# Performance work log

Measured on AMD Instinct MI355X. Metric: run time of the kernel, lower is better.

## Reference

```python
import jax, jax.numpy as jnp
import numpy as np
import math

# dims (see shape_source)
B, S, D, H, DH, W, L, F = 2, 4096, 768, 12, 64, 256, 4, 2048
DV, DID, NIN, V, CD, CS = 256, 32, 8, 4, 16, 64
DEMB = CD * CS
EPS = 1e-6
NEG = -1e9


def rmsnorm(x, w):
    y = x * jax.lax.rsqrt(jnp.mean(x * x, axis=-1, keepdims=True) + EPS)
    return y * w


def sliding_attn(q, k, v):
    # q,k,v: [B,H,S,DH]; banded attention, each query attends keys within +-W.
    nc = S // W
    q = q * (1.0 / math.sqrt(DH))
    kp = jnp.pad(k, ((0, 0), (0, 0), (W, W), (0, 0)))
    vp = jnp.pad(v, ((0, 0), (0, 0), (W, W), (0, 0)))
    idx = jnp.arange(nc)[:, None] * W + jnp.arange(3 * W)[None, :]  # [nc,3W] into padded seq
    kc = kp[:, :, idx]                                # [B,H,nc,3W,DH]
    vc = vp[:, :, idx]
    qc = q.reshape(B, H, nc, W, DH)
    scores = jnp.einsum('bhcqd,bhckd->bhcqk', qc, kc)  # [B,H,nc,W,3W]
    qpos = jnp.arange(W)[:, None]
    kpos = jnp.arange(3 * W)[None, :]
    band = jnp.abs(kpos - (qpos + W)) <= W             # [W,3W]
    kglob = jnp.arange(nc)[:, None, None] * W + kpos[None] - W  # [nc,1,3W]
    valid = band[None] & (kglob >= 0) & (kglob < S)    # [nc,W,3W]
    scores = jnp.where(valid[None, None], scores, NEG)
    probs = jax.nn.softmax(scores, axis=-1)
    out = jnp.einsum('bhcqk,bhckd->bhcqd', probs, vc)
    return out.reshape(B, H, S, DH)


def _forward(x, id, embed_table, cd_w, cd_b, wq, bq, wk, bk, wv, bv,
             attn_norm_w, ffn_norm_w, w1, b1, w2, b2, w3, b3,
             h0_w1, h0_b1, h0_w2, h0_b2, norm_head0_w, head0_w, head0_b,
             c1_w1, c1_b1, c1_w2, c1_b2, c2_w1, c2_b1, c2_w2, c2_b2,
             norm_emb_w, head1_w, head1_b):
    h = embed_table[x] * math.sqrt(DV)                         # [B,S,DV]
    bits = jnp.arange(DID - 1, -1, -1)
    idb = ((id[..., None] >> bits) & 1).astype(jnp.float32)    # decimal2binary -> [B,S,DID]
    h = jnp.concatenate([h, idb], axis=-1) @ cd_w + cd_b       # correct_dim -> [B,S,D]
    for l in range(L):
        a = rmsnorm(h, attn_norm_w[l])
        q = (a @ wq[l] + bq[l]).reshape(B, S, H, DH).transpose(0, 2, 1, 3)
        k = (a @ wk[l] + bk[l]).reshape(B, S, H, DH).transpose(0, 2, 1, 3)
        v = (a @ wv[l] + bv[l]).reshape(B, S, H, DH).transpose(0, 2, 1, 3)
        o = sliding_attn(q, k, v)                              # [B,H,S,DH]
        h = h + o.transpose(0, 2, 1, 3).reshape(B, S, D)
        f = rmsnorm(h, ffn_norm_w[l])
        h = h + (jax.nn.silu(f @ w1[l] + b1[l]) * (f @ w3[l] + b3[l])) @ w2[l] + b2[l]
    # per-token head
    t = jax.nn.silu(h @ h0_w1 + h0_b1) @ h0_w2 + h0_b2
    logits0 = rmsnorm(t, norm_head0_w) @ head0_w + head0_b     # [B,S,V]
    # compression head
    c = jax.nn.silu(h @ c1_w1 + c1_b1) @ c1_w2 + c1_b2         # [B,S,CD]
    c = c.transpose(0, 2, 1)                                    # [B,CD,S]
    c = jax.nn.silu(c @ c2_w1 + c2_b1) @ c2_w2 + c2_b2         # [B,CD,CS]
    c = c.transpose(0, 2, 1).reshape(B, DEMB)
    emb = rmsnorm(c, norm_emb_w)
    logits = (emb @ head1_w + head1_b).reshape(B, S, V)        # [B,S,V]
    return logits0, logits


def setup_inputs() -> dict:
    key = jax.random.key(0)
    ks = iter(jax.random.split(key, 80))
    def w(*shape):
        return jax.random.normal(next(ks), shape, jnp.float32) * 0.02
    z = lambda *shape: jnp.zeros(shape, jnp.float32)
    o = lambda *shape: jnp.ones(shape, jnp.float32)
    return {
        'x': jax.random.randint(next(ks), (B, S), 0, NIN),
        'id': jax.random.randint(next(ks), (B, S), 0, 2 ** 20),
        'embed_table': w(NIN, DV),
        'cd_w': w(DV + DID, D), 'cd_b': z(D),
        'wq': w(L, D, D), 'bq': z(L, D),
        'wk': w(L, D, D), 'bk': z(L, D),
        'wv': w(L, D, D), 'bv': z(L, D),
        'attn_norm_w': o(L, D), 'ffn_norm_w': o(L, D),
        'w1': w(L, D, F), 'b1': z(L, F),
        'w2': w(L, F, D), 'b2': z(L, D),
        'w3': w(L, D, F), 'b3': z(L, F),
        'h0_w1': w(D, D), 'h0_b1': z(D),
        'h0_w2': w(D, D), 'h0_b2': z(D),
        'norm_head0_w': o(D),
        'head0_w': w(D, V), 'head0_b': z(V),
        'c1_w1': w(D, D), 'c1_b1': z(D),
        'c1_w2': w(D, CD), 'c1_b2': z(CD),
        'c2_w1': w(S, S), 'c2_b1': z(S),
        'c2_w2': w(S, CS), 'c2_b2': z(CS),
        'norm_emb_w': o(DEMB),
        'head1_w': w(DEMB, S * V), 'head1_b': z(S * V),
    }


def reference(x, id, embed_table, cd_w, cd_b, wq, bq, wk, bk, wv, bv,
              attn_norm_w, ffn_norm_w, w1, b1, w2, b2, w3, b3,
              h0_w1, h0_b1, h0_w2, h0_b2, norm_head0_w, head0_w, head0_b,
              c1_w1, c1_b1, c1_w2, c1_b2, c2_w1, c2_b1, c2_w2, c2_b2,
              norm_emb_w, head1_w, head1_b):
    return _forward(x, id, embed_table, cd_w, cd_b, wq, bq, wk, bk, wv, bv,
                    attn_norm_w, ffn_norm_w, w1, b1, w2, b2, w3, b3,
                    h0_w1, h0_b1, h0_w2, h0_b2, norm_head0_w, head0_w, head0_b,
                    c1_w1, c1_b1, c1_w2, c1_b2, c2_w1, c2_b1, c2_w2, c2_b2,
                    norm_emb_w, head1_w, head1_b)
```

## Files before the change

kernel.cpp:

```cpp
#include <hip/hip_runtime.h>
#include <stdint.h>

typedef unsigned short u16;
typedef unsigned int u32;

#define SS 4096
#define NROWS 8192

__device__ __forceinline__ float bf2f(u16 u){
  union { u32 u; float f; } x; x.u = ((u32)u) << 16; return x.f;
}
__device__ __forceinline__ u16 f2bf(float f){
  union { float f; u32 u; } x; x.f = f;
  u32 r = x.u + 0x7fffu + ((x.u >> 16) & 1u);
  return (u16)(r >> 16);
}
__device__ __forceinline__ float bflo(u32 u){ union { u32 u; float f; } x; x.u = u << 16; return x.f; }
__device__ __forceinline__ float bfhi(u32 u){ union { u32 u; float f; } x; x.u = u & 0xffff0000u; return x.f; }

__device__ __forceinline__ float ldany(const void* p, size_t i, int f){
  return f ? ((const float*)p)[i] : bf2f(((const u16*)p)[i]);
}

__global__ void detect_k(const void* anw, int* flag){
  if (threadIdx.x == 0 && blockIdx.x == 0)
    flag[0] = (((const u32*)anw)[0] == 0x3F800000u) ? 1 : 0;
}

__device__ __forceinline__ void gload16(const u16* g, u16* l){
  __builtin_amdgcn_global_load_lds((const __attribute__((address_space(1))) void*)g,
                                   (__attribute__((address_space(3))) void*)l, 16, 0, 0);
}

__global__ void transpose_k(const void* __restrict__ in, size_t ioff,
                            u16* __restrict__ out, int R, int C, const int* fl){
  int f = *fl;
  __shared__ u16 t[32][33];
  int c0 = blockIdx.x * 32, r0 = blockIdx.y * 32;
  int tx = threadIdx.x & 31, ty = threadIdx.x >> 5;
  #pragma unroll
  for (int i = 0; i < 32; i += 8){
    int r = r0 + ty + i, c = c0 + tx;
    t[ty + i][tx] = (r < R && c < C) ? f2bf(ldany(in, ioff + (size_t)r * C + c, f)) : (u16)0;
  }
  __syncthreads();
  #pragma unroll
  for (int i = 0; i < 32; i += 8){
    int r = c0 + ty + i, c = r0 + tx;
    if (r < C && c < R) out[(size_t)r * R + c] = t[tx][ty + i];
  }
}

__global__ void transpose_qkv_k(const void* __restrict__ wqp, const void* __restrict__ wkp,
                                const void* __restrict__ wvp, size_t wo,
                                u16* __restrict__ out, const int* fl){
  int f = *fl;
  const void* in = (blockIdx.z == 0) ? wqp : (blockIdx.z == 1) ? wkp : wvp;
  u16* dst = out + (size_t)blockIdx.z * 768 * 768;
  __shared__ u16 t[32][33];
  int c0 = blockIdx.x * 32, r0 = blockIdx.y * 32;
  int tx = threadIdx.x & 31, ty = threadIdx.x >> 5;
  #pragma unroll
  for (int i = 0; i < 32; i += 8){
    int r = r0 + ty + i, c = c0 + tx;
    t[ty + i][tx] = f2bf(ldany(in, wo + (size_t)r * 768 + c, f));
  }
  __syncthreads();
  #pragma unroll
  for (int i = 0; i < 32; i += 8){
    int r = c0 + ty + i, c = r0 + tx;
    dst[(size_t)r * 768 + c] = t[tx][ty + i];
  }
}

__global__ void embed_k(const int* __restrict__ x, const int* __restrict__ idv,
                        const void* __restrict__ table, u16* __restrict__ xin,
                        const int* fl){
  int f = *fl;
  int row = blockIdx.x;
  int tok = x[row], idval = idv[row];
  for (int j = threadIdx.x; j < 288; j += 256){
    u16 o;
    if (j < 256) o = f2bf(ldany(table, (size_t)tok*256 + j, f) * 16.0f);
    else o = ((idval >> (31 - (j - 256))) & 1) ? (u16)0x3F80 : (u16)0;
    xin[(size_t)row * 288 + j] = o;
  }
}

__global__ __launch_bounds__(256) void rmsnormw_k(const u16* __restrict__ in,
                          const void* __restrict__ w, int woff,
                          u16* __restrict__ out, const int* fl){
  int f = *fl;
  int wave = threadIdx.x >> 6, lane = threadIdx.x & 63;
  int row = blockIdx.x*4 + wave;
  const u16* xp = in + (size_t)row * 768;
  float v[12]; float ss = 0.f;
  #pragma unroll
  for (int i = 0; i < 12; ++i){ v[i] = bf2f(xp[i*64 + lane]); ss += v[i]*v[i]; }
  #pragma unroll
  for (int o = 32; o > 0; o >>= 1) ss += __shfl_down(ss, o, 64);
  float tot = __shfl(ss, 0, 64);
  float sc = rsqrtf(tot / 768.f + 1e-6f);
  u16* op = out + (size_t)row * 768;
  #pragma unroll
  for (int i = 0; i < 12; ++i)
    op[i*64 + lane] = f2bf(v[i] * sc * ldany(w, woff + i*64 + lane, f));
}

__global__ void rmsnorm_emb_k(const float* __restrict__ in, const void* __restrict__ b2,
                              const void* __restrict__ w, float* __restrict__ out, const int* fl){
  int f = *fl;
  int row = blockIdx.x;
  const float* xp = in + (size_t)row * 1024;
  float ss = 0.f;
  for (int i = threadIdx.x; i < 1024; i += 256){
    float v = xp[i] + ldany(b2, i >> 4, f); ss += v*v;
  }
  #pragma unroll
  for (int o = 32; o > 0; o >>= 1) ss += __shfl_down(ss, o, 64);
  __shared__ float red[4];
  __shared__ float scale_s;
  int lane = threadIdx.x & 63, wv = threadIdx.x >> 6;
  if (lane == 0) red[wv] = ss;
  __syncthreads();
  if (threadIdx.x == 0){
    float tot = red[0] + red[1] + red[2] + red[3];
    scale_s = rsqrtf(tot / 1024.f + 1e-6f);
  }
  __syncthreads();
  float sc = scale_s;
  for (int i = threadIdx.x; i < 1024; i += 256)
    out[(size_t)row*1024 + i] = (xp[i] + ldany(b2, i >> 4, f)) * sc * ldany(w, i, f);
}

#define BM 128
#define BN 128
#define BK 32
#define GBN 64

typedef __attribute__((ext_vector_type(8))) __bf16 bf16x8;
typedef __attribute__((ext_vector_type(4))) float f32x4;

__device__ __forceinline__ int xcd_swz(int nwg, int orig){
  int xcd = orig & 7, loc = orig >> 3;
  int q = nwg >> 3, r = nwg & 7;
  return (xcd < r ? xcd * (q + 1) : r * (q + 1) + (xcd - r) * q) + loc;
}

__global__ __launch_bounds__(256) void gemm_bt_k(
    const u16* __restrict__ A, const u16* __restrict__ BT,
    const void* __restrict__ bias, const void* __restrict__ bias2,
    const void* __restrict__ bias3, int boff,
    u16* __restrict__ out, int M, int N, int K, int epi, const int* fl)
{
  __shared__ u16 As[2][BM*BK];
  __shared__ u16 Bs[2][BN*BK];
  const int f = *fl;
  const int tid = threadIdx.x;
  const int wave = tid >> 6, lane = tid & 63;

  const int gx = gridDim.x;
  const int nwg = gx * gridDim.y;
  const int swz = xcd_swz(nwg, blockIdx.y * gx + blockIdx.x);
  const int m0 = (swz / gx) * BM, n0 = (swz % gx) * BN;

  const int wr = (wave >> 1) * 64, wc = (wave & 1) * 64;
  const int lr = lane & 15, lq = lane >> 4;

  f32x4 acc[4][4];
  #pragma unroll
  for (int i = 0; i < 4; ++i)
    #pragma unroll
    for (int j = 0; j < 4; ++j) acc[i][j] = f32x4{0.f,0.f,0.f,0.f};

  const int r_in = lane >> 2;
  const int c_in = (lane & 3) * 8;
  const u16* gA = A  + (size_t)(m0 + wave*32 + r_in) * K + c_in;
  const u16* gB = BT + (size_t)(n0 + wave*32 + r_in) * K + c_in;

  auto stage = [&](int buf, int kt){
    u16* lA = &As[buf][wave*32*BK];
    u16* lB = &Bs[buf][wave*32*BK];
    gload16(gA + kt,        lA);
    gload16(gA + kt + 16*K, lA + 16*BK);
    gload16(gB + kt,        lB);
    gload16(gB + kt + 16*K, lB + 16*BK);
  };

  const int nk = K / BK;
  stage(0, 0);
  if (nk > 1) stage(1, BK);

  for (int t = 0; t < nk; ++t){
    if (t + 1 < nk) asm volatile("s_waitcnt vmcnt(4)" ::: "memory");
    else            asm volatile("s_waitcnt vmcnt(0)" ::: "memory");
    __builtin_amdgcn_sched_barrier(0);
    __builtin_amdgcn_s_barrier();
    __builtin_amdgcn_sched_barrier(0);

    const u16* Ab = &As[t & 1][0];
    const u16* Bb = &Bs[t & 1][0];
    bf16x8 af[4], bfr[4];
    #pragma unroll
    for (int i = 0; i < 4; ++i)
      af[i] = *(const bf16x8*)(Ab + (wr + i*16 + lr) * BK + lq*8);
    #pragma unroll
    for (int j = 0; j < 4; ++j)
      bfr[j] = *(const bf16x8*)(Bb + (wc + j*16 + lr) * BK + lq*8);
    asm volatile("s_waitcnt lgkmcnt(0)" ::: "memory");
    __builtin_amdgcn_sched_barrier(0);

    #pragma unroll
    for (int i = 0; i < 4; ++i)
      #pragma unroll
      for (int j = 0; j < 4; ++j)
        acc[i][j] = __builtin_amdgcn_mfma_f32_16x16x32_bf16(af[i], bfr[j], acc[i][j], 0, 0, 0);

    __builtin_amdgcn_sched_barrier(0);
    __builtin_amdgcn_s_barrier();
    __builtin_amdgcn_sched_barrier(0);
    if (t + 2 < nk) stage(t & 1, (t + 2) * BK);
  }

  #pragma unroll
  for (int i = 0; i < 4; ++i){
    #pragma unroll
    for (int j = 0; j < 4; ++j){
      #pragma unroll
      for (int r = 0; r < 4; ++r){
        int row = m0 + wr + i*16 + lq*4 + r;
        int col = n0 + wc + j*16 + lr;
        size_t idx = (size_t)row * N + col;
        float bb;
        if (bias3){
          if (col < 768) bb = ldany(bias, boff + col, f);
          else if (col < 1536) bb = ldany(bias2, boff + col - 768, f);
          else bb = ldany(bias3, boff + col - 1536, f);
        } else {
          bb = ldany(bias, boff + col, f);
        }
        float v = acc[i][j][r] + bb;
        if (epi == 0){
          out[idx] = f2bf(v);
        } else if (epi == 1){
          out[idx] = f2bf(v / (1.f + __expf(-v)));
        } else if (epi == 2){
          float g = bf2f(out[idx]);
          out[idx] = f2bf((g / (1.f + __expf(-g))) * v);
        } else {
          out[idx] = f2bf(bf2f(out[idx]) + v);
        }
      }
    }
  }
}

__global__ __launch_bounds__(256) void gemm_gate_k(
    const u16* __restrict__ A, const u16* __restrict__ B1T, const u16* __restrict__ B3T,
    const void* __restrict__ b1, const void* __restrict__ b3, int boff,
    u16* __restrict__ out, int M, int N, int K, const int* fl)
{
  __shared__ u16 As[2][BM*BK];
  __shared__ u16 B1s[2][GBN*BK];
  __shared__ u16 B3s[2][GBN*BK];
  const int f = *fl;
  const int tid = threadIdx.x;
  const int wave = tid >> 6, lane = tid & 63;

  const int gx = gridDim.x;
  const int nwg = gx * gridDim.y;
  const int swz = xcd_swz(nwg, blockIdx.y * gx + blockIdx.x);
  const int m0 = (swz / gx) * BM, n0 = (swz % gx) * GBN;

  const int wr = (wave >> 1) * 64, wc = (wave & 1) * 32;
  const int lr = lane & 15, lq = lane >> 4;

  f32x4 acc1[4][2], acc3[4][2];
  #pragma unroll
  for (int i = 0; i < 4; ++i)
    #pragma unroll
    for (int j = 0; j < 2; ++j){
      acc1[i][j] = f32x4{0.f,0.f,0.f,0.f};
      acc3[i][j] = f32x4{0.f,0.f,0.f,0.f};
    }

  const int r_in = lane >> 2;
  const int c_in = (lane & 3) * 8;
  const u16* gA  = A   + (size_t)(m0 + wave*32 + r_in) * K + c_in;
  const u16* gB1 = B1T + (size_t)(n0 + wave*16 + r_in) * K + c_in;
  const u16* gB3 = B3T + (size_t)(n0 + wave*16 + r_in) * K + c_in;

  auto stage = [&](int buf, int kt){
    gload16(gA + kt,        &As[buf][wave*32*BK]);
    gload16(gA + kt + 16*K, &As[buf][(wave*32 + 16)*BK]);
    gload16(gB1 + kt,       &B1s[buf][wave*16*BK]);
    gload16(gB3 + kt,       &B3s[buf][wave*16*BK]);
  };

  const int nk = K / BK;
  stage(0, 0);
  if (nk > 1) stage(1, BK);

  for (int t = 0; t < nk; ++t){
    if (t + 1 < nk) asm volatile("s_waitcnt vmcnt(4)" ::: "memory");
    else            asm volatile("s_waitcnt vmcnt(0)" ::: "memory");
    __builtin_amdgcn_sched_barrier(0);
    __builtin_amdgcn_s_barrier();
    __builtin_amdgcn_sched_barrier(0);

    const u16* Ab  = &As[t & 1][0];
    const u16* B1b = &B1s[t & 1][0];
    const u16* B3b = &B3s[t & 1][0];
    bf16x8 af[4], b1f[2], b3f[2];
    #pragma unroll
    for (int i = 0; i < 4; ++i)
      af[i] = *(const bf16x8*)(Ab + (wr + i*16 + lr) * BK + lq*8);
    #pragma unroll
    for (int j = 0; j < 2; ++j){
      b1f[j] = *(const bf16x8*)(B1b + (wc + j*16 + lr) * BK + lq*8);
      b3f[j] = *(const bf16x8*)(B3b + (wc + j*16 + lr) * BK + lq*8);
    }
    asm volatile("s_waitcnt lgkmcnt(0)" ::: "memory");
    __builtin_amdgcn_sched_barrier(0);

    #pragma unroll
    for (int i = 0; i < 4; ++i)
      #pragma unroll
      for (int j = 0; j < 2; ++j){
        acc1[i][j] = __builtin_amdgcn_mfma_f32_16x16x32_bf16(af[i], b1f[j], acc1[i][j], 0, 0, 0);
        acc3[i][j] = __builtin_amdgcn_mfma_f32_16x16x32_bf16(af[i], b3f[j], acc3[i][j], 0, 0, 0);
      }

    __builtin_amdgcn_sched_barrier(0);
    __builtin_amdgcn_s_barrier();
    __builtin_amdgcn_sched_barrier(0);
    if (t + 2 < nk) stage(t & 1, (t + 2) * BK);
  }

  #pragma unroll
  for (int i = 0; i < 4; ++i){
    #pragma unroll
    for (int j = 0; j < 2; ++j){
      #pragma unroll
      for (int r = 0; r < 4; ++r){
        int row = m0 + wr + i*16 + lq*4 + r;
        int col = n0 + wc + j*16 + lr;
        float v1 = acc1[i][j][r] + ldany(b1, boff + col, f);
        float v3 = acc3[i][j][r] + ldany(b3, boff + col, f);
        out[(size_t)row * N + col] = f2bf((v1 / (1.f + __expf(-v1))) * v3);
      }
    }
  }
}

__global__ __launch_bounds__(256) void attn_mfma_k(
    const u16* __restrict__ qkv, u16* __restrict__ h)
{
  __shared__ u16 Ks[64*72];
  __shared__ u16 Vt[64*72];
  __shared__ u16 Pl[4*32*72];
  const int qc = blockIdx.x, hh = blockIdx.y, b = blockIdx.z;
  const int q0 = qc * 128;
  const int tid = threadIdx.x, wave = tid >> 6, lane = tid & 63;
  const int lr = lane & 15, lq = lane >> 4;
  u16* Pw = Pl + wave*32*72;
  const int qrow = q0 + wave*32;

  bf16x8 qf[2][2];
  #pragma unroll
  for (int i = 0; i < 2; ++i)
    #pragma unroll
    for (int kq = 0; kq < 2; ++kq)
      qf[i][kq] = *(const bf16x8*)(qkv + (size_t)(b*SS + qrow + i*16 + lr)*2304 + hh*64 + kq*32 + lq*8);

  float m_r[2][4], l_r[2][4];
  f32x4 acc[2][4];
  #pragma unroll
  for (int i = 0; i < 2; ++i)
    #pragma unroll
    for (int r = 0; r < 4; ++r){ m_r[i][r] = -1e30f; l_r[i][r] = 0.f; }
  #pragma unroll
  for (int i = 0; i < 2; ++i)
    #pragma unroll
    for (int j = 0; j < 4; ++j) acc[i][j] = f32x4{0.f,0.f,0.f,0.f};

  for (int jt = 0; jt < 10; ++jt){
    int t0 = q0 - 256 + jt*64;
    if (t0 + 64 <= 0 || t0 >= SS) continue;

    {
      int n = tid >> 2, dp = (tid & 3) * 16;
      int kg = t0 + n;
      uint4 a = {0,0,0,0}, c = {0,0,0,0};
      if (kg >= 0 && kg < SS){
        const u16* kp = qkv + (size_t)(b*SS+kg)*2304 + 768 + hh*64 + dp;
        a = *(const uint4*)kp; c = *(const uint4*)(kp + 8);
      }
      *(uint4*)(Ks + n*72 + dp)     = a;
      *(uint4*)(Ks + n*72 + dp + 8) = c;
    }
    {
      int n = lane, dp = wave*16;
      int kg = t0 + n;
      uint4 a = {0,0,0,0}, c = {0,0,0,0};
      if (kg >= 0 && kg < SS){
        const u16* vp = qkv + (size_t)(b*SS+kg)*2304 + 1536 + hh*64 + dp;
        a = *(const uint4*)vp; c = *(const uint4*)(vp + 8);
      }
      u32 w[8] = {a.x,a.y,a.z,a.w,c.x,c.y,c.z,c.w};
      #pragma unroll
      for (int e = 0; e < 8; ++e){
        Vt[(dp + e*2    )*72 + n] = (u16)(w[e] & 0xffffu);
        Vt[(dp + e*2 + 1)*72 + n] = (u16)(w[e] >> 16);
      }
    }
    __syncthreads();

    f32x4 sc[2][4];
    #pragma unroll
    for (int i = 0; i < 2; ++i)
      #pragma unroll
      for (int j = 0; j < 4; ++j) sc[i][j] = f32x4{0.f,0.f,0.f,0.f};
    #pragma unroll
    for (int j = 0; j < 4; ++j){
      bf16x8 kfa = *(const bf16x8*)(Ks + (j*16 + lr)*72 + lq*8);
      bf16x8 kfb = *(const bf16x8*)(Ks + (j*16 + lr)*72 + 32 + lq*8);
      #pragma unroll
      for (int i = 0; i < 2; ++i){
        sc[i][j] = __builtin_amdgcn_mfma_f32_16x16x32_bf16(qf[i][0], kfa, sc[i][j], 0, 0, 0);
        sc[i][j] = __builtin_amdgcn_mfma_f32_16x16x32_bf16(qf[i][1], kfb, sc[i][j], 0, 0, 0);
      }
    }

    #pragma unroll
    for (int i = 0; i < 2; ++i){
      #pragma unroll
      for (int r = 0; r < 4; ++r){
        int qg = qrow + i*16 + lq*4 + r;
        #pragma unroll
        for (int j = 0; j < 4; ++j){
          int kg = t0 + j*16 + lr;
          float s = sc[i][j][r] * 0.125f;
          bool ok = (kg >= 0) && (kg < SS) && (kg >= qg - 256) && (kg <= qg + 256);
          sc[i][j][r] = ok ? s : -1e38f;
        }
      }
    }

    #pragma unroll
    for (int i = 0; i < 2; ++i){
      #pragma unroll
      for (int r = 0; r < 4; ++r){
        float mx = fmaxf(fmaxf(sc[i][0][r], sc[i][1][r]), fmaxf(sc[i][2][r], sc[i][3][r]));
        #pragma unroll
        for (int o = 1; o < 16; o <<= 1) mx = fmaxf(mx, __shfl_xor(mx, o, 64));
        float mn = fmaxf(m_r[i][r], mx);
        float al = __expf(m_r[i][r] - mn);
        float ps = 0.f;
        #pragma unroll
        for (int j = 0; j < 4; ++j){
          float p = __expf(sc[i][j][r] - mn);
          sc[i][j][r] = p; ps += p;
        }
        #pragma unroll
        for (int o = 1; o < 16; o <<= 1) ps += __shfl_xor(ps, o, 64);
        l_r[i][r] = l_r[i][r] * al + ps;
        m_r[i][r] = mn;
        #pragma unroll
        for (int j = 0; j < 4; ++j) acc[i][j][r] *= al;
      }
    }

    #pragma unroll
    for (int i = 0; i < 2; ++i)
      #pragma unroll
      for (int j = 0; j < 4; ++j)
        #pragma unroll
        for (int r = 0; r < 4; ++r)
          Pw[(i*16 + lq*4 + r)*72 + j*16 + lr] = f2bf(sc[i][j][r]);

    #pragma unroll
    for (int kq = 0; kq < 2; ++kq){
      bf16x8 pf0 = *(const bf16x8*)(Pw + lr*72        + kq*32 + lq*8);
      bf16x8 pf1 = *(const bf16x8*)(Pw + (16 + lr)*72 + kq*32 + lq*8);
      #pragma unroll
      for (int j = 0; j < 4; ++j){
        bf16x8 vfj = *(const bf16x8*)(Vt + (j*16 + lr)*72 + kq*32 + lq*8);
        acc[0][j] = __builtin_amdgcn_mfma_f32_16x16x32_bf16(pf0, vfj, acc[0][j], 0, 0, 0);
        acc[1][j] = __builtin_amdgcn_mfma_f32_16x16x32_bf16(pf1, vfj, acc[1][j], 0, 0, 0);
      }
    }
    __syncthreads();
  }

  #pragma unroll
  for (int i = 0; i < 2; ++i){
    #pragma unroll
    for (int r = 0; r < 4; ++r){
      float inv = 1.f / l_r[i][r];
      int qg = qrow + i*16 + lq*4 + r;
      u16* hp = h + (size_t)(b*SS + qg)*768 + hh*64;
      #pragma unroll
      for (int j = 0; j < 4; ++j){
        int d = j*16 + lr;
        hp[d] = f2bf(bf2f(hp[d]) + acc[i][j][r] * inv);
      }
    }
  }
}

template<int NN>
__global__ __launch_bounds__(256) void smalln_k(const u16* __restrict__ A, const void* __restrict__ W,
                         const void* __restrict__ bias, void* __restrict__ out,
                         const int* fl, int outmode){
  int f = *fl;
  __shared__ float Wl[NN*768];
  for (int i = threadIdx.x; i < NN*768; i += 256){
    int n = i / 768, k = i - n*768;
    Wl[i] = ldany(W, (size_t)k*NN + n, f);
  }
  __syncthreads();
  int wave = threadIdx.x >> 6, lane = threadIdx.x & 63;
  int rowbase = blockIdx.x*16 + wave*4;
  for (int r = 0; r < 4; ++r){
    int row = rowbase + r;
    const u16* ap = A + (size_t)row * 768;
    float a[12];
    #pragma unroll
    for (int i = 0; i < 12; ++i) a[i] = bf2f(ap[i*64 + lane]);
    float acc[NN];
    #pragma unroll
    for (int n = 0; n < NN; ++n) acc[n] = 0.f;
    #pragma unroll
    for (int i = 0; i < 12; ++i){
      int k = i*64 + lane;
      #pragma unroll
      for (int n = 0; n < NN; ++n) acc[n] += a[i] * Wl[n*768 + k];
    }
    float red[NN];
    #pragma unroll
    for (int n = 0; n < NN; ++n){
      float v = acc[n];
      #pragma unroll
      for (int o = 32; o > 0; o >>= 1) v += __shfl_down(v, o, 64);
      red[n] = v;
    }
    if (lane == 0){
      #pragma unroll
      for (int n = 0; n < NN; ++n){
        float v = red[n] + ldany(bias, n, f);
        size_t oi = (size_t)row*NN + n;
        if (outmode && f) ((float*)out)[oi] = v;
        else ((u16*)out)[oi] = f2bf(v);
      }
    }
  }
}

__global__ void ctrans_k(const u16* __restrict__ in, u16* __restrict__ out){
  int idx = blockIdx.x * 256 + threadIdx.x;
  int b = idx >> 16;
  int r = idx & 65535;
  int d = r >> 12, s = r & 4095;
  out[idx] = in[(size_t)(b*4096 + s)*16 + d];
}

__global__ __launch_bounds__(256) void c2mlp1_k(const u16* __restrict__ ct,
    const void* __restrict__ w, float* __restrict__ yacc, const int* fl){
  int f = *fl;
  __shared__ float Awt[64][36];
  __shared__ u16 Ws[64*128];
  int n0 = blockIdx.x * 128;
  int k0 = blockIdx.y * 512;
  int tid = threadIdx.x;
  int c4 = (tid & 31) * 4;
  int r0 = (tid >> 5) * 4;
  float acc[4][4] = {};
  for (int ks = 0; ks < 512; ks += 64){
    __syncthreads();
    {
      int mm = tid >> 3, kk8 = (tid & 7) * 8;
      uint4 av = *(const uint4*)(ct + (size_t)mm*4096 + k0 + ks + kk8);
      float fv[8] = {bflo(av.x),bfhi(av.x),bflo(av.y),bfhi(av.y),
                     bflo(av.z),bfhi(av.z),bflo(av.w),bfhi(av.w)};
      #pragma unroll
      for (int i = 0; i < 8; ++i) Awt[kk8+i][mm] = fv[i];
    }
    {
      int kk = tid >> 2, cc = (tid & 3) * 32;
      #pragma unroll
      for (int j = 0; j < 32; ++j)
        Ws[kk*128 + cc + j] = f2bf(ldany(w, (size_t)(k0+ks+kk)*4096 + n0 + cc + j, f));
    }
    __syncthreads();
    for (int kk = 0; kk < 64; ++kk){
      float4 a4 = *(const float4*)&Awt[kk][r0];
      uint2 wv = *(const uint2*)(Ws + kk*128 + c4);
      float w0 = bflo(wv.x), w1v = bfhi(wv.x), w2v = bflo(wv.y), w3v = bfhi(wv.y);
      float ar[4] = {a4.x, a4.y, a4.z, a4.w};
      #pragma unroll
      for (int r = 0; r < 4; ++r){
        acc[r][0] += ar[r]*w0;  acc[r][1] += ar[r]*w1v;
        acc[r][2] += ar[r]*w2v; acc[r][3] += ar[r]*w3v;
      }
    }
  }
  #pragma unroll
  for (int r = 0; r < 4; ++r)
    #pragma unroll
    for (int cc = 0; cc < 4; ++cc)
      atomicAdd(&yacc[(size_t)(r0+r)*4096 + n0 + c4 + cc], acc[r][cc]);
}

__global__ void silu_bias_k(const float* __restrict__ yacc, const void* __restrict__ bias,
                            u16* __restrict__ out, const int* fl){
  int f = *fl;
  int idx = blockIdx.x*256 + threadIdx.x;
  int n = idx & 4095;
  float v = yacc[idx] + ldany(bias, n, f);
  out[idx] = f2bf(v / (1.f + __expf(-v)));
}

__global__ void c2mlp2_k(const u16* __restrict__ y, const void* __restrict__ w2,
                         float* __restrict__ emb_pre, const int* fl){
  int f = *fl;
  int m = blockIdx.x, kseg = blockIdx.y;
  int col = threadIdx.x & 63, sl = threadIdx.x >> 6;
  float acc = 0.f;
  int kb = kseg*512 + sl*128;
  for (int k = kb; k < kb+128; ++k)
    acc += bf2f(y[(size_t)m*4096 + k]) * ldany(w2, (size_t)k*64 + col, f);
  __shared__ float red[256];
  red[threadIdx.x] = acc;
  __syncthreads();
  if (sl == 0){
    float t = red[col] + red[col+64] + red[col+128] + red[col+192];
    int b = m >> 4, d = m & 15;
    atomicAdd(&emb_pre[b*1024 + col*16 + d], t);
  }
}

__global__ void head1_k(const float* __restrict__ emb, const void* __restrict__ w,
                        float* __restrict__ hacc, const int* fl){
  int f = *fl;
  int n = blockIdx.x*256 + threadIdx.x;
  int k0 = blockIdx.y*256;
  float a0 = 0.f, a1 = 0.f;
  for (int k = k0; k < k0+256; ++k){
    float wv = ldany(w, (size_t)k*16384 + n, f);
    a0 += emb[k] * wv;
    a1 += emb[1024 + k] * wv;
  }
  atomicAdd(&hacc[n], a0);
  atomicAdd(&hacc[16384 + n], a1);
}

__global__ void head1fin_k(const float* __restrict__ hacc, const void* __restrict__ bias,
                           void* __restrict__ out, const int* fl){
  int f = *fl;
  int n = blockIdx.x*256 + threadIdx.x;
  float b = ldany(bias, n, f);
  float a0 = hacc[n] + b, a1 = hacc[16384 + n] + b;
  if (f){ ((float*)out)[32768 + n] = a0; ((float*)out)[49152 + n] = a1; }
  else  { ((u16*)out)[32768 + n] = f2bf(a0); ((u16*)out)[49152 + n] = f2bf(a1); }
}

extern "C" void kernel_launch(void* const* d_in, const int* in_sizes, int n_in,
                              void* d_out, int out_size, void* d_ws, size_t ws_size,
                              hipStream_t stream)
{
  const int* x   = (const int*)d_in[0];
  const int* idv = (const int*)d_in[1];
  const void* embt = d_in[2];
  const void* cd_w = d_in[3];
  const void* cd_b = d_in[4];
  const void* wq = d_in[5];
  const void* bq = d_in[6];
  const void* wk = d_in[7];
  const void* bk = d_in[8];
  const void* wv = d_in[9];
  const void* bv = d_in[10];
  const void* attn_nw = d_in[11];
  const void* ffn_nw  = d_in[12];
  const void* w1 = d_in[13];
  const void* b1 = d_in[14];
  const void* w2 = d_in[15];
  const void* b2 = d_in[16];
  const void* w3 = d_in[17];
  const void* b3 = d_in[18];
  const void* h0_w1 = d_in[19];
  const void* h0_b1 = d_in[20];
  const void* h0_w2 = d_in[21];
  const void* h0_b2 = d_in[22];
  const void* nh0_w = d_in[23];
  const void* head0_w = d_in[24];
  const void* head0_b = d_in[25];
  const void* c1_w1 = d_in[26];
  const void* c1_b1 = d_in[27];
  const void* c1_w2 = d_in[28];
  const void* c1_b2 = d_in[29];
  const void* c2_w1 = d_in[30];
  const void* c2_b1 = d_in[31];
  const void* c2_w2 = d_in[32];
  const void* c2_b2 = d_in[33];
  const void* nemb_w = d_in[34];
  const void* head1_w = d_in[35];
  const void* head1_b = d_in[36];

  char* ws = (char*)d_ws;
  size_t off = 0;
  auto alloc = [&](size_t bytes)->char*{
    char* p = ws + off; off = (off + bytes + 255) & ~(size_t)255; return p;
  };

  int*  flag  = (int*)alloc(256);
  u16*  wtbuf = (u16*)alloc((size_t)(2304+2048)*768*2);
  u16*  wt2nd = wtbuf + (size_t)2048*768;
  u16*  h     = (u16*)alloc((size_t)NROWS*768*2);
  u16*  fbuf  = (u16*)alloc((size_t)NROWS*768*2);
  char* R3    = alloc((size_t)NROWS*768*2*3);

  u16* xin  = (u16*)R3;
  u16* qkvb = (u16*)R3;
  u16* g1   = (u16*)R3;
  u16* tbuf = (u16*)R3;
  u16* gbuf = (u16*)(R3 + (size_t)NROWS*768*2);
  char* tail = R3 + (size_t)NROWS*768*2*2;
  u16* cbuf = (u16*)tail;
  u16* ctb  = (u16*)(tail + 262144);
  float* yacc = (float*)(tail + 262144*2);
  u16* ybf  = (u16*)(tail + 262144*2 + 524288);
  float* emb_pre = (float*)(tail + 262144*3 + 524288);
  float* embn    = (float*)(tail + 262144*3 + 524288 + 8192);
  float* hacc    = (float*)(tail + 262144*3 + 524288 + 16384);

  detect_k<<<1, 64, 0, stream>>>(attn_nw, flag);

  auto tr = [&](const void* src, size_t ioff, u16* dst, int R, int C){
    dim3 g((C+31)/32, (R+31)/32);
    transpose_k<<<g, 256, 0, stream>>>(src, ioff, dst, R, C, flag);
  };
  auto gemm = [&](const u16* A, const u16* BT, const void* bias, int boff,
                  u16* out_, int M, int N, int K, int epi){
    dim3 g(N/128, M/128);
    gemm_bt_k<<<g, 256, 0, stream>>>(A, BT, bias, nullptr, nullptr, boff,
                                     out_, M, N, K, epi, flag);
  };

  embed_k<<<NROWS, 256, 0, stream>>>(x, idv, embt, xin, flag);
  tr(cd_w, 0, wtbuf, 288, 768);
  gemm(xin, wtbuf, cd_b, 0, h, NROWS, 768, 288, 0);

  for (int l = 0; l < 4; ++l){
    size_t wo = (size_t)l*768*768, fo = (size_t)l*768*2048;
    rmsnormw_k<<<NROWS/4, 256, 0, stream>>>(h, attn_nw, l*768, fbuf, flag);
    transpose_qkv_k<<<dim3(24,24,3), 256, 0, stream>>>(wq, wk, wv, wo, wtbuf, flag);
    {
      dim3 g(2304/128, NROWS/128);
      gemm_bt_k<<<g, 256, 0, stream>>>(fbuf, wtbuf, bq, bk, bv, l*768,
                                       qkvb, NROWS, 2304, 768, 0, flag);
    }
    attn_mfma_k<<<dim3(32,12,2), 256, 0, stream>>>(qkvb, h);

    rmsnormw_k<<<NROWS/4, 256, 0, stream>>>(h, ffn_nw, l*768, fbuf, flag);
    tr(w1, fo, wtbuf, 768, 2048);
    tr(w3, fo, wt2nd, 768, 2048);
    {
      dim3 g(2048/GBN, NROWS/128);
      gemm_gate_k<<<g, 256, 0, stream>>>(fbuf, wtbuf, wt2nd, b1, b3, l*2048,
                                         g1, NROWS, 2048, 768, flag);
    }
    tr(w2, fo, wtbuf, 2048, 768);
    gemm(g1, wtbuf, b2, l*768, h, NROWS, 768, 2048, 3);
  }

  tr(h0_w1, 0, wtbuf, 768, 768);
  gemm(h, wtbuf, h0_b1, 0, gbuf, NROWS, 768, 768, 1);
  tr(h0_w2, 0, wtbuf, 768, 768);
  gemm(gbuf, wtbuf, h0_b2, 0, tbuf, NROWS, 768, 768, 0);
  rmsnormw_k<<<NROWS/4, 256, 0, stream>>>(tbuf, nh0_w, 0, gbuf, flag);
  smalln_k<4><<<NROWS/16, 256, 0, stream>>>(gbuf, head0_w, head0_b, d_out, flag, 1);

  tr(c1_w1, 0, wtbuf, 768, 768);
  gemm(h, wtbuf, c1_b1, 0, gbuf, NROWS, 768, 768, 1);
  smalln_k<16><<<NROWS/16, 256, 0, stream>>>(gbuf, c1_w2, c1_b2, cbuf, flag, 0);
  ctrans_k<<<512, 256, 0, stream>>>(cbuf, ctb);
  hipMemsetAsync(yacc, 0, (size_t)32*4096*4, stream);
  hipMemsetAsync(emb_pre, 0, 2*1024*4, stream);
  hipMemsetAsync(hacc, 0, (size_t)2*16384*4, stream);
  c2mlp1_k<<<dim3(32,8), 256, 0, stream>>>(ctb, c2_w1, yacc, flag);
  silu_bias_k<<<512, 256, 0, stream>>>(yacc, c2_b1, ybf, flag);
  c2mlp2_k<<<dim3(32,8), 256, 0, stream>>>(ybf, c2_w2, emb_pre, flag);
  rmsnorm_emb_k<<<2, 256, 0, stream>>>(emb_pre, c2_b2, nemb_w, embn, flag);
  head1_k<<<dim3(64,4), 256, 0, stream>>>(embn, head1_w, hacc, flag);
  head1fin_k<<<64, 256, 0, stream>>>(hacc, head1_b, d_out, flag);

  (void)in_sizes; (void)n_in; (void)out_size; (void)ws_size;
}
```

Measured before the change: 2.077 ms.

## Triple-buffer GEMM LDS stages to drop the second barrier per k-step

Both bf16 GEMM kernels go from double to triple-buffered LDS tiles. The next prefetch is issued right after the single per-iteration barrier, into a buffer no wave is still reading, so the trailing barrier can be removed. LDS reads now use inline-asm ds_read_b128, and the MFMA block runs at raised wave priority via s_setprio. This cuts one barrier per k-step and issues loads earlier, at the cost of more LDS per block, which may lower occupancy.

```diff
diff --git a/kernel.cpp b/kernel.cpp
--- a/kernel.cpp
+++ b/kernel.cpp
@@ -30,6 +30,16 @@
 __device__ __forceinline__ void gload16(const u16* g, u16* l){
   __builtin_amdgcn_global_load_lds((const __attribute__((address_space(1))) void*)g,
                                    (__attribute__((address_space(3))) void*)l, 16, 0, 0);
+}
+
+typedef __attribute__((ext_vector_type(8))) __bf16 bf16x8;
+typedef __attribute__((ext_vector_type(4))) float f32x4;
+
+__device__ __forceinline__ bf16x8 ldsr16(const u16* p){
+  bf16x8 r;
+  u32 a = (u32)(uintptr_t)(const __attribute__((address_space(3))) u16*)p;
+  asm volatile("ds_read_b128 %0, %1" : "=v"(r) : "v"(a));
+  return r;
 }
 
 __global__ void transpose_k(const void* __restrict__ in, size_t ioff,
@@ -138,14 +148,13 @@
 #define BK 32
 #define GBN 64
 
-typedef __attribute__((ext_vector_type(8))) __bf16 bf16x8;
-typedef __attribute__((ext_vector_type(4))) float f32x4;
-
 __device__ __forceinline__ int xcd_swz(int nwg, int orig){
   int xcd = orig & 7, loc = orig >> 3;
   int q = nwg >> 3, r = nwg & 7;
   return (xcd < r ? xcd * (q + 1) : r * (q + 1) + (xcd - r) * q) + loc;
 }
+
+__device__ __forceinline__ int nxt3(int i){ return i == 2 ? 0 : i + 1; }
 
 __global__ __launch_bounds__(256) void gemm_bt_k(
     const u16* __restrict__ A, const u16* __restrict__ BT,
@@ -153,9 +162,8 @@
     const void* __restrict__ bias3, int boff,
     u16* __restrict__ out, int M, int N, int K, int epi, const int* fl)
 {
-  __shared__ u16 As[2][BM*BK];
-  __shared__ u16 Bs[2][BN*BK];
-  const int f = *fl;
+  __shared__ u16 As[3][BM*BK];
+  __shared__ u16 Bs[3][BN*BK];
   const int tid = threadIdx.x;
   const int wave = tid >> 6, lane = tid & 63;
 
@@ -189,39 +197,41 @@
 
   const int nk = K / BK;
   stage(0, 0);
-  if (nk > 1) stage(1, BK);
-
+  stage(1, BK);
+
+  int cur = 0, pre = 2;
   for (int t = 0; t < nk; ++t){
     if (t + 1 < nk) asm volatile("s_waitcnt vmcnt(4)" ::: "memory");
     else            asm volatile("s_waitcnt vmcnt(0)" ::: "memory");
     __builtin_amdgcn_sched_barrier(0);
     __builtin_amdgcn_s_barrier();
     __builtin_amdgcn_sched_barrier(0);
-
-    const u16* Ab = &As[t & 1][0];
-    const u16* Bb = &Bs[t & 1][0];
+    if (t + 2 < nk) stage(pre, (t + 2) * BK);
+
+    const u16* Ab = &As[cur][0];
+    const u16* Bb = &Bs[cur][0];
     bf16x8 af[4], bfr[4];
     #pragma unroll
     for (int i = 0; i < 4; ++i)
-      af[i] = *(const bf16x8*)(Ab + (wr + i*16 + lr) * BK + lq*8);
+      af[i] = ldsr16(Ab + (wr + i*16 + lr) * BK + lq*8);
     #pragma unroll
     for (int j = 0; j < 4; ++j)
-      bfr[j] = *(const bf16x8*)(Bb + (wc + j*16 + lr) * BK + lq*8);
+      bfr[j] = ldsr16(Bb + (wc + j*16 + lr) * BK + lq*8);
     asm volatile("s_waitcnt lgkmcnt(0)" ::: "memory");
     __builtin_amdgcn_sched_barrier(0);
 
+    __builtin_amdgcn_s_setprio(1);
     #pragma unroll
     for (int i = 0; i < 4; ++i)
       #pragma unroll
       for (int j = 0; j < 4; ++j)
         acc[i][j] = __builtin_amdgcn_mfma_f32_16x16x32_bf16(af[i], bfr[j], acc[i][j], 0, 0, 0);
-
+    __builtin_amdgcn_s_setprio(0);
     __builtin_amdgcn_sched_barrier(0);
-    __builtin_amdgcn_s_barrier();
-    __builtin_amdgcn_sched_barrier(0);
-    if (t + 2 < nk) stage(t & 1, (t + 2) * BK);
-  }
-
+    cur = nxt3(cur); pre = nxt3(pre);
+  }
+
+  const int f = *fl;
   #pragma unroll
   for (int i = 0; i < 4; ++i){
     #pragma unroll
@@ -260,10 +270,9 @@
     const void* __restrict__ b1, const void* __restrict__ b3, int boff,
     u16* __restrict__ out, int M, int N, int K, const int* fl)
 {
-  __shared__ u16 As[2][BM*BK];
-  __shared__ u16 B1s[2][GBN*BK];
-  __shared__ u16 B3s[2][GBN*BK];
-  const int f = *fl;
+  __shared__ u16 As[3][BM*BK];
+  __shared__ u16 B1s[3][GBN*BK];
+  __shared__ u16 B3s[3][GBN*BK];
   const int tid = threadIdx.x;
   const int wave = tid >> 6, lane = tid & 63;
 
@@ -299,30 +308,33 @@
 
   const int nk = K / BK;
   stage(0, 0);
-  if (nk > 1) stage(1, BK);
-
+  stage(1, BK);
+
+  int cur = 0, pre = 2;
   for (int t = 0; t < nk; ++t){
     if (t + 1 < nk) asm volatile("s_waitcnt vmcnt(4)" ::: "memory");
     else            asm volatile("s_waitcnt vmcnt(0)" ::: "memory");
     __builtin_amdgcn_sched_barrier(0);
     __builtin_amdgcn_s_barrier();
     __builtin_amdgcn_sched_barrier(0);
-
-    const u16* Ab  = &As[t & 1][0];
-    const u16* B1b = &B1s[t & 1][0];
-    const u16* B3b = &B3s[t & 1][0];
+    if (t + 2 < nk) stage(pre, (t + 2) * BK);
+
+    const u16* Ab  = &As[cur][0];
+    const u16* B1b = &B1s[cur][0];
+    const u16* B3b = &B3s[cur][0];
     bf16x8 af[4], b1f[2], b3f[2];
     #pragma unroll
     for (int i = 0; i < 4; ++i)
-      af[i] = *(const bf16x8*)(Ab + (wr + i*16 + lr) * BK + lq*8);
+      af[i] = ldsr16(Ab + (wr + i*16 + lr) * BK + lq*8);
     #pragma unroll
     for (int j = 0; j < 2; ++j){
-      b1f[j] = *(const bf16x8*)(B1b + (wc + j*16 + lr) * BK + lq*8);
-      b3f[j] = *(const bf16x8*)(B3b + (wc + j*16 + lr) * BK + lq*8);
+      b1f[j] = ldsr16(B1b + (wc + j*16 + lr) * BK + lq*8);
+      b3f[j] = ldsr16(B3b + (wc + j*16 + lr) * BK + lq*8);
     }
     asm volatile("s_waitcnt lgkmcnt(0)" ::: "memory");
     __builtin_amdgcn_sched_barrier(0);
 
+    __builtin_amdgcn_s_setprio(1);
     #pragma unroll
     for (int i = 0; i < 4; ++i)
       #pragma unroll
@@ -330,13 +342,12 @@
         acc1[i][j] = __builtin_amdgcn_mfma_f32_16x16x32_bf16(af[i], b1f[j], acc1[i][j], 0, 0, 0);
         acc3[i][j] = __builtin_amdgcn_mfma_f32_16x16x32_bf16(af[i], b3f[j], acc3[i][j], 0, 0, 0);
       }
-
+    __builtin_amdgcn_s_setprio(0);
     __builtin_amdgcn_sched_barrier(0);
-    __builtin_amdgcn_s_barrier();
-    __builtin_amdgcn_sched_barrier(0);
-    if (t + 2 < nk) stage(t & 1, (t + 2) * BK);
-  }
-
+    cur = nxt3(cur); pre = nxt3(pre);
+  }
+
+  const int f = *fl;
   #pragma unroll
   for (int i = 0; i < 4; ++i){
     #pragma unroll
```

After: 1.952 ms. 6.0% less time.
